# Kernel tuning notes

Hardware: AMD Instinct MI355X
Metric: run time of the kernel (lower is better)

## Reference

```python
import jax, jax.numpy as jnp
import numpy as np

N_HEADS = 16
MASK_VAL = -50000.0  # module sets masked scores to this value (not -inf)


def setup_inputs() -> dict:
    key = jax.random.key(0)
    kq, kk, kv = jax.random.split(key, 3)
    b, n, d_model = 2, 2048, 2048
    q = jax.random.normal(kq, (b, n, d_model), dtype=jnp.float32)
    k = jax.random.normal(kk, (b, n, d_model), dtype=jnp.float32)
    v = jax.random.normal(kv, (b, n, d_model), dtype=jnp.float32)
    return {"q": q, "k": k, "v": v}


def reference(q, k, v):
    b, n, d_model = q.shape
    h = N_HEADS
    dh = d_model // h
    scale = dh ** -0.5
    # 'b n (h d) -> b h n d'
    qh = q.reshape(b, n, h, dh).transpose(0, 2, 1, 3)
    kh = k.reshape(b, n, h, dh).transpose(0, 2, 1, 3)
    vh = v.reshape(b, n, h, dh).transpose(0, 2, 1, 3)
    # dots = (q * scale) @ k^T  -> [b, h, n, n]
    dots = jnp.einsum('bhid,bhjd->bhij', qh * scale, kh)
    # per-chunk triu_indices(csz, l, offset=i*csz+1) == global causal mask j > i,
    # with masked entries SET to MASK_VAL
    i_idx = jnp.arange(n)[:, None]
    j_idx = jnp.arange(n)[None, :]
    dots = jnp.where(j_idx > i_idx, MASK_VAL, dots)
    attn = jax.nn.softmax(dots, axis=-1)
    out = jnp.einsum('bhij,bhjd->bhid', attn, vh)
    # 'b h n d -> b n (h d)'
    return out.transpose(0, 2, 1, 3).reshape(b, n, d_model)
```

## Files before the change

kernel.cpp:

```cpp
#include <hip/hip_runtime.h>
#include <hip/hip_bf16.h>

#define B_SZ   2
#define N_SEQ  2048
#define NH     16
#define DH     128
#define DM     2048
#define KVB    64
#define MASK_VAL (-50000.0f)

typedef short bf16x8 __attribute__((ext_vector_type(8)));
typedef float f32x4  __attribute__((ext_vector_type(4)));
typedef float f32x16 __attribute__((ext_vector_type(16)));
typedef unsigned u32;
typedef unsigned u32x2 __attribute__((ext_vector_type(2)));
typedef unsigned u32x4 __attribute__((ext_vector_type(4)));
typedef unsigned short ushort_t;

__device__ __forceinline__ u32 pk2(float a, float b) {
  u32 r;
  asm("v_cvt_pk_bf16_f32 %0, %1, %2" : "=v"(r) : "v"(a), "v"(b));
  return r;
}

__device__ __forceinline__ void gload_lds16(const void* g, void* l) {
  __builtin_amdgcn_global_load_lds(
      (const __attribute__((address_space(1))) unsigned int*)g,
      (__attribute__((address_space(3))) unsigned int*)l, 16, 0, 0);
}

__device__ __forceinline__ float tmax16(const f32x16& v) {
  float a = fmaxf(v[0], v[1]),  b = fmaxf(v[2], v[3]);
  float c = fmaxf(v[4], v[5]),  d = fmaxf(v[6], v[7]);
  float e = fmaxf(v[8], v[9]),  f = fmaxf(v[10], v[11]);
  float g = fmaxf(v[12], v[13]), h = fmaxf(v[14], v[15]);
  a = fmaxf(a, b); c = fmaxf(c, d); e = fmaxf(e, f); g = fmaxf(g, h);
  return fmaxf(fmaxf(a, c), fmaxf(e, g));
}
__device__ __forceinline__ float tsum16(const f32x16& v) {
  float a = v[0] + v[1],  b = v[2] + v[3];
  float c = v[4] + v[5],  d = v[6] + v[7];
  float e = v[8] + v[9],  f = v[10] + v[11];
  float g = v[12] + v[13], h = v[14] + v[15];
  a += b; c += d; e += f; g += h;
  return (a + c) + (e + g);
}

__global__ __launch_bounds__(256)
void kconv(const float* __restrict__ k, ushort_t* __restrict__ kw) {
  const int idx = blockIdx.x * 256 + threadIdx.x;
  const size_t e0 = (size_t)idx * 16;
  const int c0 = (int)(e0 & 2047);
  const int bn = (int)(e0 >> 11);
  const int b  = bn >> 11;
  const int n  = bn & 2047;
  const int h  = c0 >> 7;
  const int d0 = c0 & 127;
  const float* src = k + e0;
  float4 f0 = *(const float4*)(src);
  float4 f1 = *(const float4*)(src + 4);
  float4 f2 = *(const float4*)(src + 8);
  float4 f3 = *(const float4*)(src + 12);
  u32x4 p0, p1;
  p0[0] = pk2(f0.x, f0.y); p0[1] = pk2(f0.z, f0.w);
  p0[2] = pk2(f1.x, f1.y); p0[3] = pk2(f1.z, f1.w);
  p1[0] = pk2(f2.x, f2.y); p1[1] = pk2(f2.z, f2.w);
  p1[2] = pk2(f3.x, f3.y); p1[3] = pk2(f3.z, f3.w);
  ushort_t* dst = kw + (((size_t)(b * 16 + h) * 2048 + n) * 128 + d0);
  *(u32x4*)(dst)     = p0;
  *(u32x4*)(dst + 8) = p1;
}

__global__ __launch_bounds__(256)
void vtrans(const float* __restrict__ v, ushort_t* __restrict__ vw) {
  __shared__ __align__(16) char tile[16384];

  const int tid   = threadIdx.x;
  const int bid   = blockIdx.x;
  const int ntile = bid & 31;
  const int bh2   = bid >> 5;
  const int h     = bh2 & 15;
  const int n0    = ntile * 64;
  const float* vbase = v + (size_t)(bh2 >> 4) * N_SEQ * DM + h * DH;

  #pragma unroll
  for (int i = 0; i < 8; ++i) {
    int idx = i * 256 + tid;
    int n   = idx >> 5;
    int c4  = idx & 31;
    float4 f = *(const float4*)(vbase + (size_t)(n0 + n) * DM + c4 * 4);
    u32x2 p;
    p[0] = pk2(f.x, f.y);
    p[1] = pk2(f.z, f.w);
    int sw = (((n & 7) ^ (n >> 3)) << 4);
    *(u32x2*)(tile + n * 256 + ((8 * c4) ^ sw)) = p;
  }
  __syncthreads();

  #pragma unroll
  for (int i = 0; i < 4; ++i) {
    int idx = i * 256 + tid;
    int d   = idx >> 3;
    int nb  = idx & 7;
    u32x4 p;
    #pragma unroll
    for (int half = 0; half < 4; ++half) {
      int na = nb * 8 + half * 2;
      int nA = na, nB = na + 1;
      int swA = (((nA & 7) ^ (nA >> 3)) << 4);
      int swB = (((nB & 7) ^ (nB >> 3)) << 4);
      u32 lo = *(const ushort_t*)(tile + nA * 256 + (((d >> 2) * 8) ^ swA) + (d & 3) * 2);
      u32 hi = *(const ushort_t*)(tile + nB * 256 + (((d >> 2) * 8) ^ swB) + (d & 3) * 2);
      p[half] = lo | (hi << 16);
    }
    ushort_t* dst = vw + (((size_t)bh2 * 128 + d) * 2048 + n0 + nb * 8);
    *(u32x4*)(dst) = p;
  }
}

__global__ __launch_bounds__(512, 1)
void attn_fwd(const float* __restrict__ q, const ushort_t* __restrict__ kw,
              const ushort_t* __restrict__ vw, float* __restrict__ out) {
  __shared__ __align__(16) char  ldsK[2 * 64 * 256];
  __shared__ __align__(16) char  ldsVT[2 * 128 * 128];
  __shared__ __align__(16) float ldsA[8 * 32];

  const int tid  = threadIdx.x;
  const int lane = tid & 63;
  const int w    = tid >> 6;
  const int h    = lane >> 5;
  const int il   = lane & 31;

  const int bid = blockIdx.x;
  const int bh  = bid & 31;
  const int kk  = bid >> 5;
  const int b   = bh >> 4;
  const int hd  = bh & 15;
  const int qt_w = 2 * kk + (w < 4 ? 1 : 0);
  const int wq0  = qt_w * 128 + (w & 3) * 32;
  const int irow = wq0 + il;

  const float scale = 0.08838834764831845f;

  const ushort_t* kb16 = kw + (size_t)(b * 16 + hd) * N_SEQ * DH;
  const ushort_t* vt16 = vw + (size_t)(b * 16 + hd) * DH * N_SEQ;

  auto stage = [&](int jt, int buf) {
    char* K  = ldsK  + buf * 16384;
    char* VT = ldsVT + buf * 16384;
    const ushort_t* kt = kb16 + (size_t)jt * DH;
    #pragma unroll
    for (int c = 0; c < 2; ++c) {
      int ch  = c * 512 + tid;
      int r   = ch >> 4;
      int pos = ch & 15;
      const ushort_t* g = kt + (size_t)r * DH + ((pos ^ (r & 7)) * 8);
      gload_lds16(g, K + ch * 16);
    }
    #pragma unroll
    for (int c = 0; c < 2; ++c) {
      int ch  = c * 512 + tid;
      int d   = ch >> 3;
      int pos = ch & 7;
      const ushort_t* g = vt16 + (size_t)d * N_SEQ + jt + ((pos ^ (d & 7)) * 8);
      gload_lds16(g, VT + ch * 16);
    }
  };

  bf16x8 qf[8];
  {
    const float* qr = q + ((size_t)b * N_SEQ + irow) * DM + hd * DH + h * 8;
    #pragma unroll
    for (int s = 0; s < 8; ++s) {
      float4 a = *(const float4*)(qr + s * 16);
      float4 c = *(const float4*)(qr + s * 16 + 4);
      u32x4 t4;
      t4[0] = pk2(a.x * scale, a.y * scale);
      t4[1] = pk2(a.z * scale, a.w * scale);
      t4[2] = pk2(c.x * scale, c.y * scale);
      t4[3] = pk2(c.z * scale, c.w * scale);
      qf[s] = __builtin_bit_cast(bf16x8, t4);
    }
  }

  float m_ = -INFINITY, ll = 0.f;
  f32x16 o[4];
  #pragma unroll
  for (int dt = 0; dt < 4; ++dt)
    #pragma unroll
    for (int r = 0; r < 16; ++r) o[dt][r] = 0.f;

  const int kswz = (il & 7) << 4;
  const int nt = 4 * kk + 4;

  stage(0, 0);
  __syncthreads();

  for (int t = 0; t < nt; ++t) {
    const int jt  = t * KVB;
    const int cur = t & 1;
    if (t + 1 < nt) stage(jt + KVB, cur ^ 1);

    if (jt <= wq0 + 31) {
      char* K  = ldsK  + cur * 16384;
      char* VT = ldsVT + cur * 16384;
      const bool act1 = (jt + 32 <= wq0 + 31);

      f32x16 sc0 = {0,0,0,0,0,0,0,0,0,0,0,0,0,0,0,0};
      f32x16 sc1 = {0,0,0,0,0,0,0,0,0,0,0,0,0,0,0,0};
      __builtin_amdgcn_s_setprio(1);
      #pragma unroll
      for (int s = 0; s < 8; ++s) {
        bf16x8 kf0 = *(const bf16x8*)(K + il * 256 + ((s * 32 + h * 16) ^ kswz));
        sc0 = __builtin_amdgcn_mfma_f32_32x32x16_bf16(kf0, qf[s], sc0, 0, 0, 0);
      }
      if (act1) {
        #pragma unroll
        for (int s = 0; s < 8; ++s) {
          bf16x8 kf1 = *(const bf16x8*)(K + (32 + il) * 256 + ((s * 32 + h * 16) ^ kswz));
          sc1 = __builtin_amdgcn_mfma_f32_32x32x16_bf16(kf1, qf[s], sc1, 0, 0, 0);
        }
      }
      __builtin_amdgcn_s_setprio(0);

      if (jt + 31 > wq0) {
        #pragma unroll
        for (int r = 0; r < 16; ++r) {
          int j = jt + (r & 3) + 8 * (r >> 2) + 4 * h;
          sc0[r] = (j > irow) ? MASK_VAL : sc0[r];
        }
      }
      if (act1 && (jt + 63 > wq0)) {
        #pragma unroll
        for (int r = 0; r < 16; ++r) {
          int j = jt + 32 + (r & 3) + 8 * (r >> 2) + 4 * h;
          sc1[r] = (j > irow) ? MASK_VAL : sc1[r];
        }
      }

      float pmax = tmax16(sc0);
      if (act1) pmax = fmaxf(pmax, tmax16(sc1));
      pmax = fmaxf(pmax, __shfl_xor(pmax, 32));

      if (!__all(pmax <= m_ + 8.f)) {
        const float mnew = fmaxf(m_, pmax);
        const float alpha = __expf(m_ - mnew);
        ll *= alpha;
        m_ = mnew;
        ldsA[w * 32 + il] = alpha;
        f32x4 av[4];
        #pragma unroll
        for (int m = 0; m < 4; ++m)
          av[m] = *(const f32x4*)(ldsA + w * 32 + 8 * m + 4 * h);
        #pragma unroll
        for (int dt = 0; dt < 4; ++dt)
          #pragma unroll
          for (int m = 0; m < 4; ++m)
            #pragma unroll
            for (int r2 = 0; r2 < 4; ++r2)
              o[dt][m * 4 + r2] *= av[m][r2];
      }

      #pragma unroll
      for (int r = 0; r < 16; ++r) sc0[r] = __expf(sc0[r] - m_);
      if (act1) {
        #pragma unroll
        for (int r = 0; r < 16; ++r) sc1[r] = __expf(sc1[r] - m_);
      }
      float rs = tsum16(sc0);
      if (act1) rs += tsum16(sc1);
      rs += __shfl_xor(rs, 32);
      ll += rs;

      bf16x8 pa0[2], pa1[2];
      #pragma unroll
      for (int ss = 0; ss < 2; ++ss) {
        u32 w0 = pk2(sc0[8 * ss + 0], sc0[8 * ss + 1]);
        u32 w1 = pk2(sc0[8 * ss + 2], sc0[8 * ss + 3]);
        u32 w2 = pk2(sc0[8 * ss + 4], sc0[8 * ss + 5]);
        u32 w3 = pk2(sc0[8 * ss + 6], sc0[8 * ss + 7]);
        asm volatile("v_permlane32_swap_b32 %0, %1" : "+v"(w0), "+v"(w2));
        asm volatile("v_permlane32_swap_b32 %0, %1" : "+v"(w1), "+v"(w3));
        u32x4 t4 = {w0, w1, w2, w3};
        pa0[ss] = __builtin_bit_cast(bf16x8, t4);
      }
      if (act1) {
        #pragma unroll
        for (int ss = 0; ss < 2; ++ss) {
          u32 w0 = pk2(sc1[8 * ss + 0], sc1[8 * ss + 1]);
          u32 w1 = pk2(sc1[8 * ss + 2], sc1[8 * ss + 3]);
          u32 w2 = pk2(sc1[8 * ss + 4], sc1[8 * ss + 5]);
          u32 w3 = pk2(sc1[8 * ss + 6], sc1[8 * ss + 7]);
          asm volatile("v_permlane32_swap_b32 %0, %1" : "+v"(w0), "+v"(w2));
          asm volatile("v_permlane32_swap_b32 %0, %1" : "+v"(w1), "+v"(w3));
          u32x4 t4 = {w0, w1, w2, w3};
          pa1[ss] = __builtin_bit_cast(bf16x8, t4);
        }
      }

      __builtin_amdgcn_s_setprio(1);
      #pragma unroll
      for (int dt = 0; dt < 4; ++dt) {
        const int drow = dt * 32 + il;
        char* vrow = VT + drow * 128;
        bf16x8 vf0 = *(const bf16x8*)(vrow + ((0 * 32 + 16 * h) ^ kswz));
        o[dt] = __builtin_amdgcn_mfma_f32_32x32x16_bf16(pa0[0], vf0, o[dt], 0, 0, 0);
        bf16x8 vf1 = *(const bf16x8*)(vrow + ((1 * 32 + 16 * h) ^ kswz));
        o[dt] = __builtin_amdgcn_mfma_f32_32x32x16_bf16(pa0[1], vf1, o[dt], 0, 0, 0);
        if (act1) {
          bf16x8 vf2 = *(const bf16x8*)(vrow + ((2 * 32 + 16 * h) ^ kswz));
          o[dt] = __builtin_amdgcn_mfma_f32_32x32x16_bf16(pa1[0], vf2, o[dt], 0, 0, 0);
          bf16x8 vf3 = *(const bf16x8*)(vrow + ((3 * 32 + 16 * h) ^ kswz));
          o[dt] = __builtin_amdgcn_mfma_f32_32x32x16_bf16(pa1[1], vf3, o[dt], 0, 0, 0);
        }
      }
      __builtin_amdgcn_s_setprio(0);
    }

    if (t + 1 < nt) __syncthreads();
  }

  ldsA[w * 32 + il] = 1.0f / ll;
  f32x4 iv[4];
  #pragma unroll
  for (int m = 0; m < 4; ++m)
    iv[m] = *(const f32x4*)(ldsA + w * 32 + 8 * m + 4 * h);

  float* ob = out + ((size_t)b * N_SEQ + wq0) * DM + hd * DH;
  #pragma unroll
  for (int dt = 0; dt < 4; ++dt) {
    #pragma unroll
    for (int m = 0; m < 4; ++m) {
      #pragma unroll
      for (int r2 = 0; r2 < 4; ++r2) {
        int i_loc = 8 * m + 4 * h + r2;
        ob[(size_t)i_loc * DM + dt * 32 + il] = o[dt][m * 4 + r2] * iv[m][r2];
      }
    }
  }
}

extern "C" void kernel_launch(void* const* d_in, const int* in_sizes, int n_in,
                              void* d_out, int out_size, void* d_ws, size_t ws_size,
                              hipStream_t stream) {
  const float* q = (const float*)d_in[0];
  const float* k = (const float*)d_in[1];
  const float* v = (const float*)d_in[2];
  float* out = (float*)d_out;

  ushort_t* kw = (ushort_t*)d_ws;
  ushort_t* vw = kw + (size_t)B_SZ * NH * N_SEQ * DH;

  kconv <<<2048, 256, 0, stream>>>(k, kw);
  vtrans<<<1024, 256, 0, stream>>>(v, vw);
  attn_fwd<<<256, 512, 0, stream>>>(q, kw, vw, out);
}
```

Before: 106.5 us.

## Use small 2-wave blocks with 64-row query tiles and balanced tile ordering

The attention kernel moves from 256 blocks of 512 threads, each covering two 128-row query tiles with double-buffered K/V staging, to 1024 blocks of 128 threads, each covering one 64-row query tile with a single LDS buffer. Blocks are assigned query tiles in a zigzag order so long and short causal workloads interleave across the grid, and the QK^T product uses two independent accumulator chains to shorten MFMA dependency stalls. The aim is better load balance and more resident blocks per CU for latency hiding. In exchange, K/V tiles are reloaded by many more blocks, and the single buffer places a load-then-sync barrier on every iteration with no prefetch overlap.

```diff
diff --git a/kernel.cpp b/kernel.cpp
--- a/kernel.cpp
+++ b/kernel.cpp
@@ -118,12 +118,12 @@
   }
 }
 
-__global__ __launch_bounds__(512, 1)
+__global__ __launch_bounds__(128, 2)
 void attn_fwd(const float* __restrict__ q, const ushort_t* __restrict__ kw,
               const ushort_t* __restrict__ vw, float* __restrict__ out) {
-  __shared__ __align__(16) char  ldsK[2 * 64 * 256];
-  __shared__ __align__(16) char  ldsVT[2 * 128 * 128];
-  __shared__ __align__(16) float ldsA[8 * 32];
+  __shared__ __align__(16) char  ldsK[64 * 256];
+  __shared__ __align__(16) char  ldsVT[128 * 128];
+  __shared__ __align__(16) float ldsA[2 * 32];
 
   const int tid  = threadIdx.x;
   const int lane = tid & 63;
@@ -132,12 +132,15 @@
   const int il   = lane & 31;
 
   const int bid = blockIdx.x;
-  const int bh  = bid & 31;
-  const int kk  = bid >> 5;
+  const int j   = bid & 255;
+  const int s   = bid >> 8;
+  const int bh  = j & 31;
+  const int a   = j >> 5;
+  const int qt  = (s == 0) ? (31 - a) : (s == 1) ? (16 + a)
+                : (s == 2) ? (15 - a) : a;
   const int b   = bh >> 4;
   const int hd  = bh & 15;
-  const int qt_w = 2 * kk + (w < 4 ? 1 : 0);
-  const int wq0  = qt_w * 128 + (w & 3) * 32;
+  const int wq0 = qt * 64 + w * 32;
   const int irow = wq0 + il;
 
   const float scale = 0.08838834764831845f;
@@ -145,25 +148,23 @@
   const ushort_t* kb16 = kw + (size_t)(b * 16 + hd) * N_SEQ * DH;
   const ushort_t* vt16 = vw + (size_t)(b * 16 + hd) * DH * N_SEQ;
 
-  auto stage = [&](int jt, int buf) {
-    char* K  = ldsK  + buf * 16384;
-    char* VT = ldsVT + buf * 16384;
+  auto stage = [&](int jt) {
     const ushort_t* kt = kb16 + (size_t)jt * DH;
     #pragma unroll
-    for (int c = 0; c < 2; ++c) {
-      int ch  = c * 512 + tid;
+    for (int c = 0; c < 8; ++c) {
+      int ch  = c * 128 + tid;
       int r   = ch >> 4;
       int pos = ch & 15;
       const ushort_t* g = kt + (size_t)r * DH + ((pos ^ (r & 7)) * 8);
-      gload_lds16(g, K + ch * 16);
-    }
-    #pragma unroll
-    for (int c = 0; c < 2; ++c) {
-      int ch  = c * 512 + tid;
+      gload_lds16(g, ldsK + ch * 16);
+    }
+    #pragma unroll
+    for (int c = 0; c < 8; ++c) {
+      int ch  = c * 128 + tid;
       int d   = ch >> 3;
       int pos = ch & 7;
       const ushort_t* g = vt16 + (size_t)d * N_SEQ + jt + ((pos ^ (d & 7)) * 8);
-      gload_lds16(g, VT + ch * 16);
+      gload_lds16(g, ldsVT + ch * 16);
     }
   };
 
@@ -171,15 +172,15 @@
   {
     const float* qr = q + ((size_t)b * N_SEQ + irow) * DM + hd * DH + h * 8;
     #pragma unroll
-    for (int s = 0; s < 8; ++s) {
-      float4 a = *(const float4*)(qr + s * 16);
-      float4 c = *(const float4*)(qr + s * 16 + 4);
+    for (int s2 = 0; s2 < 8; ++s2) {
+      float4 a2 = *(const float4*)(qr + s2 * 16);
+      float4 c2 = *(const float4*)(qr + s2 * 16 + 4);
       u32x4 t4;
-      t4[0] = pk2(a.x * scale, a.y * scale);
-      t4[1] = pk2(a.z * scale, a.w * scale);
-      t4[2] = pk2(c.x * scale, c.y * scale);
-      t4[3] = pk2(c.z * scale, c.w * scale);
-      qf[s] = __builtin_bit_cast(bf16x8, t4);
+      t4[0] = pk2(a2.x * scale, a2.y * scale);
+      t4[1] = pk2(a2.z * scale, a2.w * scale);
+      t4[2] = pk2(c2.x * scale, c2.y * scale);
+      t4[3] = pk2(c2.z * scale, c2.w * scale);
+      qf[s2] = __builtin_bit_cast(bf16x8, t4);
     }
   }
 
@@ -191,133 +192,137 @@
     for (int r = 0; r < 16; ++r) o[dt][r] = 0.f;
 
   const int kswz = (il & 7) << 4;
-  const int nt = 4 * kk + 4;
-
-  stage(0, 0);
-  __syncthreads();
+  const int nt = qt + 1;
 
   for (int t = 0; t < nt; ++t) {
-    const int jt  = t * KVB;
-    const int cur = t & 1;
-    if (t + 1 < nt) stage(jt + KVB, cur ^ 1);
-
-    if (jt <= wq0 + 31) {
-      char* K  = ldsK  + cur * 16384;
-      char* VT = ldsVT + cur * 16384;
-      const bool act1 = (jt + 32 <= wq0 + 31);
-
-      f32x16 sc0 = {0,0,0,0,0,0,0,0,0,0,0,0,0,0,0,0};
-      f32x16 sc1 = {0,0,0,0,0,0,0,0,0,0,0,0,0,0,0,0};
-      __builtin_amdgcn_s_setprio(1);
-      #pragma unroll
-      for (int s = 0; s < 8; ++s) {
-        bf16x8 kf0 = *(const bf16x8*)(K + il * 256 + ((s * 32 + h * 16) ^ kswz));
-        sc0 = __builtin_amdgcn_mfma_f32_32x32x16_bf16(kf0, qf[s], sc0, 0, 0, 0);
-      }
-      if (act1) {
-        #pragma unroll
-        for (int s = 0; s < 8; ++s) {
-          bf16x8 kf1 = *(const bf16x8*)(K + (32 + il) * 256 + ((s * 32 + h * 16) ^ kswz));
-          sc1 = __builtin_amdgcn_mfma_f32_32x32x16_bf16(kf1, qf[s], sc1, 0, 0, 0);
-        }
-      }
-      __builtin_amdgcn_s_setprio(0);
-
-      if (jt + 31 > wq0) {
-        #pragma unroll
-        for (int r = 0; r < 16; ++r) {
-          int j = jt + (r & 3) + 8 * (r >> 2) + 4 * h;
-          sc0[r] = (j > irow) ? MASK_VAL : sc0[r];
-        }
-      }
-      if (act1 && (jt + 63 > wq0)) {
-        #pragma unroll
-        for (int r = 0; r < 16; ++r) {
-          int j = jt + 32 + (r & 3) + 8 * (r >> 2) + 4 * h;
-          sc1[r] = (j > irow) ? MASK_VAL : sc1[r];
-        }
-      }
-
-      float pmax = tmax16(sc0);
-      if (act1) pmax = fmaxf(pmax, tmax16(sc1));
-      pmax = fmaxf(pmax, __shfl_xor(pmax, 32));
-
-      if (!__all(pmax <= m_ + 8.f)) {
-        const float mnew = fmaxf(m_, pmax);
-        const float alpha = __expf(m_ - mnew);
-        ll *= alpha;
-        m_ = mnew;
-        ldsA[w * 32 + il] = alpha;
-        f32x4 av[4];
+    const int jt = t * KVB;
+    if (t) __syncthreads();
+    stage(jt);
+    __syncthreads();
+
+    const bool act1 = (jt + 32 <= wq0 + 31);
+
+    f32x16 sc0 = {0,0,0,0,0,0,0,0,0,0,0,0,0,0,0,0};
+    f32x16 sc0b = {0,0,0,0,0,0,0,0,0,0,0,0,0,0,0,0};
+    f32x16 sc1 = {0,0,0,0,0,0,0,0,0,0,0,0,0,0,0,0};
+    f32x16 sc1b = {0,0,0,0,0,0,0,0,0,0,0,0,0,0,0,0};
+    __builtin_amdgcn_s_setprio(1);
+    #pragma unroll
+    for (int s2 = 0; s2 < 4; ++s2) {
+      bf16x8 kf0 = *(const bf16x8*)(ldsK + il * 256 + ((s2 * 32 + h * 16) ^ kswz));
+      sc0 = __builtin_amdgcn_mfma_f32_32x32x16_bf16(kf0, qf[s2], sc0, 0, 0, 0);
+      bf16x8 kf0b = *(const bf16x8*)(ldsK + il * 256 + (((s2 + 4) * 32 + h * 16) ^ kswz));
+      sc0b = __builtin_amdgcn_mfma_f32_32x32x16_bf16(kf0b, qf[s2 + 4], sc0b, 0, 0, 0);
+    }
+    if (act1) {
+      #pragma unroll
+      for (int s2 = 0; s2 < 4; ++s2) {
+        bf16x8 kf1 = *(const bf16x8*)(ldsK + (32 + il) * 256 + ((s2 * 32 + h * 16) ^ kswz));
+        sc1 = __builtin_amdgcn_mfma_f32_32x32x16_bf16(kf1, qf[s2], sc1, 0, 0, 0);
+        bf16x8 kf1b = *(const bf16x8*)(ldsK + (32 + il) * 256 + (((s2 + 4) * 32 + h * 16) ^ kswz));
+        sc1b = __builtin_amdgcn_mfma_f32_32x32x16_bf16(kf1b, qf[s2 + 4], sc1b, 0, 0, 0);
+      }
+    }
+    __builtin_amdgcn_s_setprio(0);
+    #pragma unroll
+    for (int r = 0; r < 16; ++r) sc0[r] += sc0b[r];
+    if (act1) {
+      #pragma unroll
+      for (int r = 0; r < 16; ++r) sc1[r] += sc1b[r];
+    }
+
+    if (jt + 31 > wq0) {
+      #pragma unroll
+      for (int r = 0; r < 16; ++r) {
+        int jj = jt + (r & 3) + 8 * (r >> 2) + 4 * h;
+        sc0[r] = (jj > irow) ? MASK_VAL : sc0[r];
+      }
+    }
+    if (act1 && (jt + 63 > wq0)) {
+      #pragma unroll
+      for (int r = 0; r < 16; ++r) {
+        int jj = jt + 32 + (r & 3) + 8 * (r >> 2) + 4 * h;
+        sc1[r] = (jj > irow) ? MASK_VAL : sc1[r];
+      }
+    }
+
+    float pmax = tmax16(sc0);
+    if (act1) pmax = fmaxf(pmax, tmax16(sc1));
+    pmax = fmaxf(pmax, __shfl_xor(pmax, 32));
+
+    if (!__all(pmax <= m_ + 8.f)) {
+      const float mnew = fmaxf(m_, pmax);
+      const float alpha = __expf(m_ - mnew);
+      ll *= alpha;
+      m_ = mnew;
+      ldsA[w * 32 + il] = alpha;
+      f32x4 av[4];
+      #pragma unroll
+      for (int m = 0; m < 4; ++m)
+        av[m] = *(const f32x4*)(ldsA + w * 32 + 8 * m + 4 * h);
+      #pragma unroll
+      for (int dt = 0; dt < 4; ++dt)
         #pragma unroll
         for (int m = 0; m < 4; ++m)
-          av[m] = *(const f32x4*)(ldsA + w * 32 + 8 * m + 4 * h);
-        #pragma unroll
-        for (int dt = 0; dt < 4; ++dt)
           #pragma unroll
-          for (int m = 0; m < 4; ++m)
-            #pragma unroll
-            for (int r2 = 0; r2 < 4; ++r2)
-              o[dt][m * 4 + r2] *= av[m][r2];
-      }
-
-      #pragma unroll
-      for (int r = 0; r < 16; ++r) sc0[r] = __expf(sc0[r] - m_);
-      if (act1) {
-        #pragma unroll
-        for (int r = 0; r < 16; ++r) sc1[r] = __expf(sc1[r] - m_);
-      }
-      float rs = tsum16(sc0);
-      if (act1) rs += tsum16(sc1);
-      rs += __shfl_xor(rs, 32);
-      ll += rs;
-
-      bf16x8 pa0[2], pa1[2];
+          for (int r2 = 0; r2 < 4; ++r2)
+            o[dt][m * 4 + r2] *= av[m][r2];
+    }
+
+    #pragma unroll
+    for (int r = 0; r < 16; ++r) sc0[r] = __expf(sc0[r] - m_);
+    if (act1) {
+      #pragma unroll
+      for (int r = 0; r < 16; ++r) sc1[r] = __expf(sc1[r] - m_);
+    }
+    float rs = tsum16(sc0);
+    if (act1) rs += tsum16(sc1);
+    rs += __shfl_xor(rs, 32);
+    ll += rs;
+
+    bf16x8 pa0[2], pa1[2];
+    #pragma unroll
+    for (int ss = 0; ss < 2; ++ss) {
+      u32 w0 = pk2(sc0[8 * ss + 0], sc0[8 * ss + 1]);
+      u32 w1 = pk2(sc0[8 * ss + 2], sc0[8 * ss + 3]);
+      u32 w2 = pk2(sc0[8 * ss + 4], sc0[8 * ss + 5]);
+      u32 w3 = pk2(sc0[8 * ss + 6], sc0[8 * ss + 7]);
+      asm volatile("v_permlane32_swap_b32 %0, %1" : "+v"(w0), "+v"(w2));
+      asm volatile("v_permlane32_swap_b32 %0, %1" : "+v"(w1), "+v"(w3));
+      u32x4 t4 = {w0, w1, w2, w3};
+      pa0[ss] = __builtin_bit_cast(bf16x8, t4);
+    }
+    if (act1) {
       #pragma unroll
       for (int ss = 0; ss < 2; ++ss) {
-        u32 w0 = pk2(sc0[8 * ss + 0], sc0[8 * ss + 1]);
-        u32 w1 = pk2(sc0[8 * ss + 2], sc0[8 * ss + 3]);
-        u32 w2 = pk2(sc0[8 * ss + 4], sc0[8 * ss + 5]);
-        u32 w3 = pk2(sc0[8 * ss + 6], sc0[8 * ss + 7]);
+        u32 w0 = pk2(sc1[8 * ss + 0], sc1[8 * ss + 1]);
+        u32 w1 = pk2(sc1[8 * ss + 2], sc1[8 * ss + 3]);
+        u32 w2 = pk2(sc1[8 * ss + 4], sc1[8 * ss + 5]);
+        u32 w3 = pk2(sc1[8 * ss + 6], sc1[8 * ss + 7]);
         asm volatile("v_permlane32_swap_b32 %0, %1" : "+v"(w0), "+v"(w2));
         asm volatile("v_permlane32_swap_b32 %0, %1" : "+v"(w1), "+v"(w3));
         u32x4 t4 = {w0, w1, w2, w3};
-        pa0[ss] = __builtin_bit_cast(bf16x8, t4);
-      }
+        pa1[ss] = __builtin_bit_cast(bf16x8, t4);
+      }
+    }
+
+    __builtin_amdgcn_s_setprio(1);
+    #pragma unroll
+    for (int dt = 0; dt < 4; ++dt) {
+      const int drow = dt * 32 + il;
+      char* vrow = ldsVT + drow * 128;
+      bf16x8 vf0 = *(const bf16x8*)(vrow + ((0 * 32 + 16 * h) ^ kswz));
+      o[dt] = __builtin_amdgcn_mfma_f32_32x32x16_bf16(pa0[0], vf0, o[dt], 0, 0, 0);
+      bf16x8 vf1 = *(const bf16x8*)(vrow + ((1 * 32 + 16 * h) ^ kswz));
+      o[dt] = __builtin_amdgcn_mfma_f32_32x32x16_bf16(pa0[1], vf1, o[dt], 0, 0, 0);
       if (act1) {
-        #pragma unroll
-        for (int ss = 0; ss < 2; ++ss) {
-          u32 w0 = pk2(sc1[8 * ss + 0], sc1[8 * ss + 1]);
-          u32 w1 = pk2(sc1[8 * ss + 2], sc1[8 * ss + 3]);
-          u32 w2 = pk2(sc1[8 * ss + 4], sc1[8 * ss + 5]);
-          u32 w3 = pk2(sc1[8 * ss + 6], sc1[8 * ss + 7]);
-          asm volatile("v_permlane32_swap_b32 %0, %1" : "+v"(w0), "+v"(w2));
-          asm volatile("v_permlane32_swap_b32 %0, %1" : "+v"(w1), "+v"(w3));
-          u32x4 t4 = {w0, w1, w2, w3};
-          pa1[ss] = __builtin_bit_cast(bf16x8, t4);
-        }
-      }
-
-      __builtin_amdgcn_s_setprio(1);
-      #pragma unroll
-      for (int dt = 0; dt < 4; ++dt) {
-        const int drow = dt * 32 + il;
-        char* vrow = VT + drow * 128;
-        bf16x8 vf0 = *(const bf16x8*)(vrow + ((0 * 32 + 16 * h) ^ kswz));
-        o[dt] = __builtin_amdgcn_mfma_f32_32x32x16_bf16(pa0[0], vf0, o[dt], 0, 0, 0);
-        bf16x8 vf1 = *(const bf16x8*)(vrow + ((1 * 32 + 16 * h) ^ kswz));
-        o[dt] = __builtin_amdgcn_mfma_f32_32x32x16_bf16(pa0[1], vf1, o[dt], 0, 0, 0);
-        if (act1) {
-          bf16x8 vf2 = *(const bf16x8*)(vrow + ((2 * 32 + 16 * h) ^ kswz));
-          o[dt] = __builtin_amdgcn_mfma_f32_32x32x16_bf16(pa1[0], vf2, o[dt], 0, 0, 0);
-          bf16x8 vf3 = *(const bf16x8*)(vrow + ((3 * 32 + 16 * h) ^ kswz));
-          o[dt] = __builtin_amdgcn_mfma_f32_32x32x16_bf16(pa1[1], vf3, o[dt], 0, 0, 0);
-        }
-      }
-      __builtin_amdgcn_s_setprio(0);
-    }
-
-    if (t + 1 < nt) __syncthreads();
+        bf16x8 vf2 = *(const bf16x8*)(vrow + ((2 * 32 + 16 * h) ^ kswz));
+        o[dt] = __builtin_amdgcn_mfma_f32_32x32x16_bf16(pa1[0], vf2, o[dt], 0, 0, 0);
+        bf16x8 vf3 = *(const bf16x8*)(vrow + ((3 * 32 + 16 * h) ^ kswz));
+        o[dt] = __builtin_amdgcn_mfma_f32_32x32x16_bf16(pa1[1], vf3, o[dt], 0, 0, 0);
+      }
+    }
+    __builtin_amdgcn_s_setprio(0);
   }
 
   ldsA[w * 32 + il] = 1.0f / ll;
@@ -353,5 +358,5 @@
 
   kconv <<<2048, 256, 0, stream>>>(k, kw);
   vtrans<<<1024, 256, 0, stream>>>(v, vw);
-  attn_fwd<<<256, 512, 0, stream>>>(q, kw, vw, out);
-}
+  attn_fwd<<<1024, 128, 0, stream>>>(q, kw, vw, out);
+}
```

Result: slower. 119.5 us (+12.2%).

## Pair low and high causal query chunks per wave to balance attention work

Applied to the files above, without the earlier changes.

Each block now has 4 waves, and each wave handles two 32-row query chunks, one low (cL) and one mirrored high (63-cL), so every wave does about the same amount of causal work. Each staged K/V tile is reused by both chunks, which removes the per-block imbalance between waves on the diagonal. The cost is twice the accumulator registers per wave (two O tiles and two Q fragment sets) and half as many waves per block to hide latency.

```diff
diff --git a/kernel.cpp b/kernel.cpp
--- a/kernel.cpp
+++ b/kernel.cpp
@@ -118,12 +118,12 @@
   }
 }
 
-__global__ __launch_bounds__(512, 1)
+__global__ __launch_bounds__(256, 1)
 void attn_fwd(const float* __restrict__ q, const ushort_t* __restrict__ kw,
               const ushort_t* __restrict__ vw, float* __restrict__ out) {
   __shared__ __align__(16) char  ldsK[2 * 64 * 256];
   __shared__ __align__(16) char  ldsVT[2 * 128 * 128];
-  __shared__ __align__(16) float ldsA[8 * 32];
+  __shared__ __align__(16) float ldsA[4 * 2 * 32];
 
   const int tid  = threadIdx.x;
   const int lane = tid & 63;
@@ -133,12 +133,16 @@
 
   const int bid = blockIdx.x;
   const int bh  = bid & 31;
-  const int kk  = bid >> 5;
+  const int s   = bid >> 5;
   const int b   = bh >> 4;
   const int hd  = bh & 15;
-  const int qt_w = 2 * kk + (w < 4 ? 1 : 0);
-  const int wq0  = qt_w * 128 + (w & 3) * 32;
-  const int irow = wq0 + il;
+
+  const int cL = s * 4 + w;
+  const int cH = 63 - cL;
+  const int lq0 = cL * 32;
+  const int hq0 = cH * 32;
+  const int irowL = lq0 + il;
+  const int irowH = hq0 + il;
 
   const float scale = 0.08838834764831845f;
 
@@ -150,16 +154,16 @@
     char* VT = ldsVT + buf * 16384;
     const ushort_t* kt = kb16 + (size_t)jt * DH;
     #pragma unroll
-    for (int c = 0; c < 2; ++c) {
-      int ch  = c * 512 + tid;
+    for (int c = 0; c < 4; ++c) {
+      int ch  = c * 256 + tid;
       int r   = ch >> 4;
       int pos = ch & 15;
       const ushort_t* g = kt + (size_t)r * DH + ((pos ^ (r & 7)) * 8);
       gload_lds16(g, K + ch * 16);
     }
     #pragma unroll
-    for (int c = 0; c < 2; ++c) {
-      int ch  = c * 512 + tid;
+    for (int c = 0; c < 4; ++c) {
+      int ch  = c * 256 + tid;
       int d   = ch >> 3;
       int pos = ch & 7;
       const ushort_t* g = vt16 + (size_t)d * N_SEQ + jt + ((pos ^ (d & 7)) * 8);
@@ -167,166 +171,187 @@
     }
   };
 
-  bf16x8 qf[8];
+  bf16x8 qfL[8], qfH[8];
   {
-    const float* qr = q + ((size_t)b * N_SEQ + irow) * DM + hd * DH + h * 8;
-    #pragma unroll
-    for (int s = 0; s < 8; ++s) {
-      float4 a = *(const float4*)(qr + s * 16);
-      float4 c = *(const float4*)(qr + s * 16 + 4);
+    const float* qrL = q + ((size_t)b * N_SEQ + irowL) * DM + hd * DH + h * 8;
+    const float* qrH = q + ((size_t)b * N_SEQ + irowH) * DM + hd * DH + h * 8;
+    #pragma unroll
+    for (int s2 = 0; s2 < 8; ++s2) {
+      float4 a2 = *(const float4*)(qrL + s2 * 16);
+      float4 c2 = *(const float4*)(qrL + s2 * 16 + 4);
       u32x4 t4;
-      t4[0] = pk2(a.x * scale, a.y * scale);
-      t4[1] = pk2(a.z * scale, a.w * scale);
-      t4[2] = pk2(c.x * scale, c.y * scale);
-      t4[3] = pk2(c.z * scale, c.w * scale);
-      qf[s] = __builtin_bit_cast(bf16x8, t4);
-    }
-  }
-
-  float m_ = -INFINITY, ll = 0.f;
-  f32x16 o[4];
+      t4[0] = pk2(a2.x * scale, a2.y * scale);
+      t4[1] = pk2(a2.z * scale, a2.w * scale);
+      t4[2] = pk2(c2.x * scale, c2.y * scale);
+      t4[3] = pk2(c2.z * scale, c2.w * scale);
+      qfL[s2] = __builtin_bit_cast(bf16x8, t4);
+      float4 a3 = *(const float4*)(qrH + s2 * 16);
+      float4 c3 = *(const float4*)(qrH + s2 * 16 + 4);
+      u32x4 t5;
+      t5[0] = pk2(a3.x * scale, a3.y * scale);
+      t5[1] = pk2(a3.z * scale, a3.w * scale);
+      t5[2] = pk2(c3.x * scale, c3.y * scale);
+      t5[3] = pk2(c3.z * scale, c3.w * scale);
+      qfH[s2] = __builtin_bit_cast(bf16x8, t5);
+    }
+  }
+
+  float mL = -INFINITY, llL = 0.f, mH = -INFINITY, llH = 0.f;
+  f32x16 oL[4], oH[4];
   #pragma unroll
   for (int dt = 0; dt < 4; ++dt)
     #pragma unroll
-    for (int r = 0; r < 16; ++r) o[dt][r] = 0.f;
+    for (int r = 0; r < 16; ++r) { oL[dt][r] = 0.f; oH[dt][r] = 0.f; }
 
   const int kswz = (il & 7) << 4;
-  const int nt = 4 * kk + 4;
-
-  stage(0, 0);
-  __syncthreads();
-
-  for (int t = 0; t < nt; ++t) {
-    const int jt  = t * KVB;
-    const int cur = t & 1;
-    if (t + 1 < nt) stage(jt + KVB, cur ^ 1);
-
-    if (jt <= wq0 + 31) {
-      char* K  = ldsK  + cur * 16384;
-      char* VT = ldsVT + cur * 16384;
-      const bool act1 = (jt + 32 <= wq0 + 31);
-
-      f32x16 sc0 = {0,0,0,0,0,0,0,0,0,0,0,0,0,0,0,0};
-      f32x16 sc1 = {0,0,0,0,0,0,0,0,0,0,0,0,0,0,0,0};
-      __builtin_amdgcn_s_setprio(1);
-      #pragma unroll
-      for (int s = 0; s < 8; ++s) {
-        bf16x8 kf0 = *(const bf16x8*)(K + il * 256 + ((s * 32 + h * 16) ^ kswz));
-        sc0 = __builtin_amdgcn_mfma_f32_32x32x16_bf16(kf0, qf[s], sc0, 0, 0, 0);
-      }
-      if (act1) {
-        #pragma unroll
-        for (int s = 0; s < 8; ++s) {
-          bf16x8 kf1 = *(const bf16x8*)(K + (32 + il) * 256 + ((s * 32 + h * 16) ^ kswz));
-          sc1 = __builtin_amdgcn_mfma_f32_32x32x16_bf16(kf1, qf[s], sc1, 0, 0, 0);
-        }
-      }
-      __builtin_amdgcn_s_setprio(0);
-
-      if (jt + 31 > wq0) {
-        #pragma unroll
-        for (int r = 0; r < 16; ++r) {
-          int j = jt + (r & 3) + 8 * (r >> 2) + 4 * h;
-          sc0[r] = (j > irow) ? MASK_VAL : sc0[r];
-        }
-      }
-      if (act1 && (jt + 63 > wq0)) {
-        #pragma unroll
-        for (int r = 0; r < 16; ++r) {
-          int j = jt + 32 + (r & 3) + 8 * (r >> 2) + 4 * h;
-          sc1[r] = (j > irow) ? MASK_VAL : sc1[r];
-        }
-      }
-
-      float pmax = tmax16(sc0);
-      if (act1) pmax = fmaxf(pmax, tmax16(sc1));
-      pmax = fmaxf(pmax, __shfl_xor(pmax, 32));
-
-      if (!__all(pmax <= m_ + 8.f)) {
-        const float mnew = fmaxf(m_, pmax);
-        const float alpha = __expf(m_ - mnew);
-        ll *= alpha;
-        m_ = mnew;
-        ldsA[w * 32 + il] = alpha;
-        f32x4 av[4];
+
+  const int cH0 = 63 - s * 4;
+  const int ntB = (((cH0) * 32 + 31) >> 6) + 1;
+
+  auto process = [&](const bf16x8* qf, int wq0, int irow, float& m_, float& ll,
+                     f32x16* o, int jt, char* K, char* VT, int aslot) {
+    const bool act1 = (jt + 32 <= wq0 + 31);
+    f32x16 sc0 = {0,0,0,0,0,0,0,0,0,0,0,0,0,0,0,0};
+    f32x16 sc1 = {0,0,0,0,0,0,0,0,0,0,0,0,0,0,0,0};
+    __builtin_amdgcn_s_setprio(1);
+    #pragma unroll
+    for (int s2 = 0; s2 < 8; ++s2) {
+      bf16x8 kf0 = *(const bf16x8*)(K + il * 256 + ((s2 * 32 + h * 16) ^ kswz));
+      sc0 = __builtin_amdgcn_mfma_f32_32x32x16_bf16(kf0, qf[s2], sc0, 0, 0, 0);
+    }
+    if (act1) {
+      #pragma unroll
+      for (int s2 = 0; s2 < 8; ++s2) {
+        bf16x8 kf1 = *(const bf16x8*)(K + (32 + il) * 256 + ((s2 * 32 + h * 16) ^ kswz));
+        sc1 = __builtin_amdgcn_mfma_f32_32x32x16_bf16(kf1, qf[s2], sc1, 0, 0, 0);
+      }
+    }
+    __builtin_amdgcn_s_setprio(0);
+
+    if (jt + 31 > wq0) {
+      #pragma unroll
+      for (int r = 0; r < 16; ++r) {
+        int jj = jt + (r & 3) + 8 * (r >> 2) + 4 * h;
+        sc0[r] = (jj > irow) ? MASK_VAL : sc0[r];
+      }
+    }
+    if (act1 && (jt + 63 > wq0)) {
+      #pragma unroll
+      for (int r = 0; r < 16; ++r) {
+        int jj = jt + 32 + (r & 3) + 8 * (r >> 2) + 4 * h;
+        sc1[r] = (jj > irow) ? MASK_VAL : sc1[r];
+      }
+    }
+
+    float pmax = tmax16(sc0);
+    if (act1) pmax = fmaxf(pmax, tmax16(sc1));
+    pmax = fmaxf(pmax, __shfl_xor(pmax, 32));
+
+    if (!__all(pmax <= m_ + 8.f)) {
+      const float mnew = fmaxf(m_, pmax);
+      const float alpha = __expf(m_ - mnew);
+      ll *= alpha;
+      m_ = mnew;
+      ldsA[aslot + il] = alpha;
+      f32x4 av[4];
+      #pragma unroll
+      for (int m = 0; m < 4; ++m)
+        av[m] = *(const f32x4*)(ldsA + aslot + 8 * m + 4 * h);
+      #pragma unroll
+      for (int dt = 0; dt < 4; ++dt)
         #pragma unroll
         for (int m = 0; m < 4; ++m)
-          av[m] = *(const f32x4*)(ldsA + w * 32 + 8 * m + 4 * h);
-        #pragma unroll
-        for (int dt = 0; dt < 4; ++dt)
           #pragma unroll
-          for (int m = 0; m < 4; ++m)
-            #pragma unroll
-            for (int r2 = 0; r2 < 4; ++r2)
-              o[dt][m * 4 + r2] *= av[m][r2];
-      }
-
-      #pragma unroll
-      for (int r = 0; r < 16; ++r) sc0[r] = __expf(sc0[r] - m_);
-      if (act1) {
-        #pragma unroll
-        for (int r = 0; r < 16; ++r) sc1[r] = __expf(sc1[r] - m_);
-      }
-      float rs = tsum16(sc0);
-      if (act1) rs += tsum16(sc1);
-      rs += __shfl_xor(rs, 32);
-      ll += rs;
-
-      bf16x8 pa0[2], pa1[2];
+          for (int r2 = 0; r2 < 4; ++r2)
+            o[dt][m * 4 + r2] *= av[m][r2];
+    }
+
+    #pragma unroll
+    for (int r = 0; r < 16; ++r) sc0[r] = __expf(sc0[r] - m_);
+    if (act1) {
+      #pragma unroll
+      for (int r = 0; r < 16; ++r) sc1[r] = __expf(sc1[r] - m_);
+    }
+    float rs = tsum16(sc0);
+    if (act1) rs += tsum16(sc1);
+    rs += __shfl_xor(rs, 32);
+    ll += rs;
+
+    bf16x8 pa0[2], pa1[2];
+    #pragma unroll
+    for (int ss = 0; ss < 2; ++ss) {
+      u32 w0 = pk2(sc0[8 * ss + 0], sc0[8 * ss + 1]);
+      u32 w1 = pk2(sc0[8 * ss + 2], sc0[8 * ss + 3]);
+      u32 w2 = pk2(sc0[8 * ss + 4], sc0[8 * ss + 5]);
+      u32 w3 = pk2(sc0[8 * ss + 6], sc0[8 * ss + 7]);
+      asm volatile("v_permlane32_swap_b32 %0, %1" : "+v"(w0), "+v"(w2));
+      asm volatile("v_permlane32_swap_b32 %0, %1" : "+v"(w1), "+v"(w3));
+      u32x4 t4 = {w0, w1, w2, w3};
+      pa0[ss] = __builtin_bit_cast(bf16x8, t4);
+    }
+    if (act1) {
       #pragma unroll
       for (int ss = 0; ss < 2; ++ss) {
-        u32 w0 = pk2(sc0[8 * ss + 0], sc0[8 * ss + 1]);
-        u32 w1 = pk2(sc0[8 * ss + 2], sc0[8 * ss + 3]);
-        u32 w2 = pk2(sc0[8 * ss + 4], sc0[8 * ss + 5]);
-        u32 w3 = pk2(sc0[8 * ss + 6], sc0[8 * ss + 7]);
+        u32 w0 = pk2(sc1[8 * ss + 0], sc1[8 * ss + 1]);
+        u32 w1 = pk2(sc1[8 * ss + 2], sc1[8 * ss + 3]);
+        u32 w2 = pk2(sc1[8 * ss + 4], sc1[8 * ss + 5]);
+        u32 w3 = pk2(sc1[8 * ss + 6], sc1[8 * ss + 7]);
         asm volatile("v_permlane32_swap_b32 %0, %1" : "+v"(w0), "+v"(w2));
         asm volatile("v_permlane32_swap_b32 %0, %1" : "+v"(w1), "+v"(w3));
         u32x4 t4 = {w0, w1, w2, w3};
-        pa0[ss] = __builtin_bit_cast(bf16x8, t4);
-      }
+        pa1[ss] = __builtin_bit_cast(bf16x8, t4);
+      }
+    }
+
+    __builtin_amdgcn_s_setprio(1);
+    #pragma unroll
+    for (int dt = 0; dt < 4; ++dt) {
+      const int drow = dt * 32 + il;
+      char* vrow = VT + drow * 128;
+      bf16x8 vf0 = *(const bf16x8*)(vrow + ((0 * 32 + 16 * h) ^ kswz));
+      o[dt] = __builtin_amdgcn_mfma_f32_32x32x16_bf16(pa0[0], vf0, o[dt], 0, 0, 0);
+      bf16x8 vf1 = *(const bf16x8*)(vrow + ((1 * 32 + 16 * h) ^ kswz));
+      o[dt] = __builtin_amdgcn_mfma_f32_32x32x16_bf16(pa0[1], vf1, o[dt], 0, 0, 0);
       if (act1) {
-        #pragma unroll
-        for (int ss = 0; ss < 2; ++ss) {
-          u32 w0 = pk2(sc1[8 * ss + 0], sc1[8 * ss + 1]);
-          u32 w1 = pk2(sc1[8 * ss + 2], sc1[8 * ss + 3]);
-          u32 w2 = pk2(sc1[8 * ss + 4], sc1[8 * ss + 5]);
-          u32 w3 = pk2(sc1[8 * ss + 6], sc1[8 * ss + 7]);
-          asm volatile("v_permlane32_swap_b32 %0, %1" : "+v"(w0), "+v"(w2));
-          asm volatile("v_permlane32_swap_b32 %0, %1" : "+v"(w1), "+v"(w3));
-          u32x4 t4 = {w0, w1, w2, w3};
-          pa1[ss] = __builtin_bit_cast(bf16x8, t4);
-        }
-      }
-
-      __builtin_amdgcn_s_setprio(1);
-      #pragma unroll
-      for (int dt = 0; dt < 4; ++dt) {
-        const int drow = dt * 32 + il;
-        char* vrow = VT + drow * 128;
-        bf16x8 vf0 = *(const bf16x8*)(vrow + ((0 * 32 + 16 * h) ^ kswz));
-        o[dt] = __builtin_amdgcn_mfma_f32_32x32x16_bf16(pa0[0], vf0, o[dt], 0, 0, 0);
-        bf16x8 vf1 = *(const bf16x8*)(vrow + ((1 * 32 + 16 * h) ^ kswz));
-        o[dt] = __builtin_amdgcn_mfma_f32_32x32x16_bf16(pa0[1], vf1, o[dt], 0, 0, 0);
-        if (act1) {
-          bf16x8 vf2 = *(const bf16x8*)(vrow + ((2 * 32 + 16 * h) ^ kswz));
-          o[dt] = __builtin_amdgcn_mfma_f32_32x32x16_bf16(pa1[0], vf2, o[dt], 0, 0, 0);
-          bf16x8 vf3 = *(const bf16x8*)(vrow + ((3 * 32 + 16 * h) ^ kswz));
-          o[dt] = __builtin_amdgcn_mfma_f32_32x32x16_bf16(pa1[1], vf3, o[dt], 0, 0, 0);
-        }
-      }
-      __builtin_amdgcn_s_setprio(0);
-    }
-
-    if (t + 1 < nt) __syncthreads();
-  }
-
-  ldsA[w * 32 + il] = 1.0f / ll;
-  f32x4 iv[4];
-  #pragma unroll
-  for (int m = 0; m < 4; ++m)
-    iv[m] = *(const f32x4*)(ldsA + w * 32 + 8 * m + 4 * h);
-
-  float* ob = out + ((size_t)b * N_SEQ + wq0) * DM + hd * DH;
+        bf16x8 vf2 = *(const bf16x8*)(vrow + ((2 * 32 + 16 * h) ^ kswz));
+        o[dt] = __builtin_amdgcn_mfma_f32_32x32x16_bf16(pa1[0], vf2, o[dt], 0, 0, 0);
+        bf16x8 vf3 = *(const bf16x8*)(vrow + ((3 * 32 + 16 * h) ^ kswz));
+        o[dt] = __builtin_amdgcn_mfma_f32_32x32x16_bf16(pa1[1], vf3, o[dt], 0, 0, 0);
+      }
+    }
+    __builtin_amdgcn_s_setprio(0);
+  };
+
+  stage(0, 0);
+  __syncthreads();
+
+  for (int t = 0; t < ntB; ++t) {
+    const int jt  = t * KVB;
+    const int cur = t & 1;
+    if (t + 1 < ntB) stage(jt + KVB, cur ^ 1);
+
+    char* K  = ldsK  + cur * 16384;
+    char* VT = ldsVT + cur * 16384;
+
+    if (jt <= hq0 + 31)
+      process(qfH, hq0, irowH, mH, llH, oH, jt, K, VT, (w * 2 + 0) * 32);
+    if (jt <= lq0 + 31)
+      process(qfL, lq0, irowL, mL, llL, oL, jt, K, VT, (w * 2 + 1) * 32);
+
+    if (t + 1 < ntB) __syncthreads();
+  }
+
+  ldsA[(w * 2 + 0) * 32 + il] = 1.0f / llH;
+  ldsA[(w * 2 + 1) * 32 + il] = 1.0f / llL;
+  f32x4 ivH[4], ivL[4];
+  #pragma unroll
+  for (int m = 0; m < 4; ++m) {
+    ivH[m] = *(const f32x4*)(ldsA + (w * 2 + 0) * 32 + 8 * m + 4 * h);
+    ivL[m] = *(const f32x4*)(ldsA + (w * 2 + 1) * 32 + 8 * m + 4 * h);
+  }
+
+  float* obH = out + ((size_t)b * N_SEQ + hq0) * DM + hd * DH;
+  float* obL = out + ((size_t)b * N_SEQ + lq0) * DM + hd * DH;
   #pragma unroll
   for (int dt = 0; dt < 4; ++dt) {
     #pragma unroll
@@ -334,7 +359,8 @@
       #pragma unroll
       for (int r2 = 0; r2 < 4; ++r2) {
         int i_loc = 8 * m + 4 * h + r2;
-        ob[(size_t)i_loc * DM + dt * 32 + il] = o[dt][m * 4 + r2] * iv[m][r2];
+        obH[(size_t)i_loc * DM + dt * 32 + il] = oH[dt][m * 4 + r2] * ivH[m][r2];
+        obL[(size_t)i_loc * DM + dt * 32 + il] = oL[dt][m * 4 + r2] * ivL[m][r2];
       }
     }
   }
@@ -353,5 +379,5 @@
 
   kconv <<<2048, 256, 0, stream>>>(k, kw);
   vtrans<<<1024, 256, 0, stream>>>(v, vw);
-  attn_fwd<<<256, 512, 0, stream>>>(q, kw, vw, out);
-}
+  attn_fwd<<<256, 256, 0, stream>>>(q, kw, vw, out);
+}
```

New measurement: 119.4 us. 12.1% more time.
